# Kernel tuning notes

Hardware: AMD Instinct MI355X
Metric: run time of the kernel (lower is better)

Reference implementation:

```python
import jax, jax.numpy as jnp
import numpy as np

N_HEADS = 4
D_HEAD = 64
SCALE = D_HEAD ** -0.5


def setup_inputs() -> dict:
    key = jax.random.key(0)
    k0, k1, k2, k3, k4 = jax.random.split(key, 5)
    C = 256
    return {
        "x": jax.random.normal(k0, (32, C, 32, 32), dtype=jnp.float32),
        "W_qkv": jax.random.normal(k1, (C, 3 * N_HEADS * D_HEAD), dtype=jnp.float32) * 0.02,
        "b_qkv": jax.random.normal(k2, (3 * N_HEADS * D_HEAD,), dtype=jnp.float32) * 0.02,
        "W_out": jax.random.normal(k3, (C, C), dtype=jnp.float32) * 0.02,
        "b_out": jax.random.normal(k4, (C,), dtype=jnp.float32) * 0.02,
    }


def reference(x, W_qkv, b_qkv, W_out, b_out):
    b, c, h, w = x.shape
    # [B, C, H, W] -> [B, S, C], S = H*W  (NOTE: GroupNorm is defined in the
    # original module but never applied in forward; we match that exactly.)
    xs = x.reshape(b, c, h * w).transpose(0, 2, 1)
    qkv = (xs @ W_qkv + b_qkv).reshape(b, -1, N_HEADS, 3 * D_HEAD)
    q, k, v = jnp.split(qkv, 3, axis=-1)  # each [B, S, H, D]
    scores = jnp.einsum('bihd,bjhd->bijh', q, k) * SCALE  # [B, S, S, H]
    attn = jax.nn.softmax(scores, axis=2)  # softmax over key index j
    res = jnp.einsum('bijh,bjhd->bihd', attn, v).reshape(b, -1, N_HEADS * D_HEAD)
    res = res @ W_out + b_out + xs
    return res.transpose(0, 2, 1).reshape(b, c, h, w)
```

## Files before the change

kernel.cpp:

```cpp
#include <hip/hip_runtime.h>

#define NH 4
#define DH 64
#define SS 1024
#define CC 256
#define BB 32

typedef __attribute__((ext_vector_type(8))) short short8;
typedef __attribute__((ext_vector_type(4))) float floatx4;
typedef __attribute__((ext_vector_type(16))) float floatx16;
typedef __attribute__((ext_vector_type(2))) unsigned uint2v;

#define MFMA16(a, b, c) __builtin_amdgcn_mfma_f32_16x16x32_bf16(a, b, c, 0, 0, 0)
#define MFMA32(a, b, c) __builtin_amdgcn_mfma_f32_32x32x16_bf16(a, b, c, 0, 0, 0)

#define QSCALE 0.18033688011112042f

__device__ __forceinline__ short f2bf(float f) {
    union { float f; unsigned u; } v; v.f = f;
    unsigned r = (v.u + 0x7fffu + ((v.u >> 16) & 1u)) >> 16;
    return (short)r;
}
__device__ __forceinline__ unsigned bfrn(float f) {
    union { float f; unsigned u; } v; v.f = f;
    return (v.u + 0x7fffu + ((v.u >> 16) & 1u)) >> 16;
}
__device__ __forceinline__ unsigned pk2_trunc(float a, float b) {
    union { float f; unsigned u; } ua, ub; ua.f = a; ub.f = b;
    return (ua.u >> 16) | (ub.u & 0xFFFF0000u);
}
__device__ __forceinline__ unsigned pk2_rn(float a, float b) {
    return bfrn(a) | (bfrn(b) << 16);
}

__global__ __launch_bounds__(256) void k_prep(const float* __restrict__ x,
                                              const float* __restrict__ Wqkv,
                                              const float* __restrict__ Wout,
                                              short* __restrict__ xs,
                                              short* __restrict__ Wqkv_t,
                                              short* __restrict__ Wout_t) {
    int bid = blockIdx.x;
    if (bid < 2048) {
        __shared__ float tile[64][65];
        int b = bid >> 6;
        int s0 = ((bid >> 2) & 15) * 64;
        int c0 = (bid & 3) * 64;
        int t = threadIdx.x;
        int tx = t & 63, ty = t >> 6;
        for (int i = 0; i < 16; ++i) {
            int c = ty + i * 4;
            tile[tx][c] = x[((b * CC) + (c0 + c)) * SS + s0 + tx];
        }
        __syncthreads();
        for (int i = 0; i < 8; ++i) {
            int s = (t >> 5) + i * 8;
            int cp = (t & 31) * 2;
            short2 v;
            v.x = f2bf(tile[s][cp]);
            v.y = f2bf(tile[s][cp + 1]);
            *(short2*)(&xs[((b * SS) + (s0 + s)) * CC + c0 + cp]) = v;
        }
    } else {
        int idx = (bid - 2048) * 256 + threadIdx.x;
        if (idx < 768 * 256) {
            int n = idx >> 8, k = idx & 255;
            Wqkv_t[idx] = f2bf(Wqkv[k * 768 + n]);
        } else {
            int j = idx - 768 * 256;
            int c = j >> 8, k = j & 255;
            Wout_t[j] = f2bf(Wout[k * 256 + c]);
        }
    }
}

__global__ __launch_bounds__(256) void k_qkv(const short* __restrict__ xs,
                                             const short* __restrict__ Wt,
                                             const float* __restrict__ bqkv,
                                             short* __restrict__ qtw,
                                             short* __restrict__ kw,
                                             short* __restrict__ vtw) {
    __shared__ short smem[10240];
    short* As = smem;
    short* Bs = smem + 5120;
    int bid = blockIdx.x;
    int idx = bid >> 3;
    int m0 = ((bid & 7) * 32 + idx / 6) * 128;
    int n0 = (idx % 6) * 128;
    int t = threadIdx.x;
    int lane = t & 63, wid = t >> 6;
    int wr = wid >> 1, wc = wid & 1;
    int c16 = lane & 15, qd = lane >> 4;

    floatx4 acc[4][4] = {};
    short8 pa[2], pb[2];

    for (int j = 0; j < 2; ++j) {
        int id = j * 256 + t, row = id >> 2, cc = id & 3;
        pa[j] = *(const short8*)(&xs[(m0 + row) * CC + cc * 8]);
        pb[j] = *(const short8*)(&Wt[(n0 + row) * CC + cc * 8]);
    }
    for (int kt = 0; kt < 8; ++kt) {
        if (kt) __syncthreads();
        for (int j = 0; j < 2; ++j) {
            int id = j * 256 + t, row = id >> 2, cc = id & 3;
            *(short8*)(&As[row * 40 + cc * 8]) = pa[j];
            *(short8*)(&Bs[row * 40 + cc * 8]) = pb[j];
        }
        __syncthreads();
        if (kt < 7) {
            for (int j = 0; j < 2; ++j) {
                int id = j * 256 + t, row = id >> 2, cc = id & 3;
                pa[j] = *(const short8*)(&xs[(m0 + row) * CC + (kt + 1) * 32 + cc * 8]);
                pb[j] = *(const short8*)(&Wt[(n0 + row) * CC + (kt + 1) * 32 + cc * 8]);
            }
        }
        short8 av[4], bv[4];
        for (int i = 0; i < 4; ++i) {
            av[i] = *(const short8*)(&As[(wr * 64 + i * 16 + c16) * 40 + qd * 8]);
            bv[i] = *(const short8*)(&Bs[(wc * 64 + i * 16 + c16) * 40 + qd * 8]);
        }
        for (int mi = 0; mi < 4; ++mi)
            for (int ni = 0; ni < 4; ++ni)
                acc[mi][ni] = MFMA16(av[mi], bv[ni], acc[mi][ni]);
    }

    int b = m0 >> 10, sbase = m0 & 1023;
    int seg = (n0 >> 6) + wc;
    int sel = seg % 3, h = seg / 3;
    int bh = b * NH + h;
    float bias4[4];
    for (int ni = 0; ni < 4; ++ni)
        bias4[ni] = bqkv[n0 + wc * 64 + ni * 16 + c16];

    if (sel != 1) {
        float sc = (sel == 0) ? QSCALE : 1.f;
        short* dst = (sel == 0) ? qtw : vtw;
        for (int ni = 0; ni < 4; ++ni) {
            int d = ni * 16 + c16;
            for (int mi = 0; mi < 4; ++mi) {
                int s = sbase + wr * 64 + mi * 16 + qd * 4;
                uint2 ow;
                ow.x = pk2_rn((acc[mi][ni][0] + bias4[ni]) * sc,
                              (acc[mi][ni][1] + bias4[ni]) * sc);
                ow.y = pk2_rn((acc[mi][ni][2] + bias4[ni]) * sc,
                              (acc[mi][ni][3] + bias4[ni]) * sc);
                *(uint2*)(&dst[(size_t)(bh * DH + d) * SS + s]) = ow;
            }
        }
    }

    int seg0 = n0 >> 6;
    int kseg = (seg0 % 3 == 1) ? seg0 : (((seg0 + 1) % 3 == 1) ? seg0 + 1 : -1);
    if (kseg >= 0) {
        short* Kt = smem;
        __syncthreads();
        if (seg == kseg) {
            for (int mi = 0; mi < 4; ++mi)
                for (int ni = 0; ni < 4; ++ni)
                    for (int r = 0; r < 4; ++r)
                        Kt[(wr * 64 + mi * 16 + qd * 4 + r) * 72 + ni * 16 + c16] =
                            f2bf(acc[mi][ni][r] + bias4[ni]);
        }
        __syncthreads();
        int bhk = b * NH + kseg / 3;
        int srow = t >> 1, dh = (t & 1) * 32;
        short* gdst = &kw[(size_t)(bhk * SS + sbase + srow) * DH + dh];
        const short* lsrc = &Kt[srow * 72 + dh];
        for (int k = 0; k < 4; ++k)
            *(short8*)(gdst + k * 8) = *(const short8*)(lsrc + k * 8);
    }
}

__global__ __launch_bounds__(256) void k_attn(const short* __restrict__ qtw,
                                              const short* __restrict__ kw,
                                              const short* __restrict__ vtw,
                                              short* __restrict__ res) {
    __shared__ __align__(16) short Ks[64 * 72];
    __shared__ __align__(16) short Vts[64 * 72];
    int bid = blockIdx.x;
    int q0 = (bid >> 7) * 128;
    int bh = bid & 127;
    int t = threadIdx.x;
    int lane = t & 63, w = t >> 6;
    int l31 = lane & 31, hi = lane >> 5;
    const short* qp = qtw + (size_t)bh * DH * SS;
    const short* kp = kw + (size_t)bh * SS * DH;
    const short* vp = vtw + (size_t)bh * DH * SS;

    short8 qfrag[4];
    {
        int s = q0 + w * 32 + l31;
        for (int kd = 0; kd < 4; ++kd) {
            short8 q;
            for (int e = 0; e < 8; ++e)
                q[e] = qp[(size_t)(kd * 16 + hi * 8 + e) * SS + s];
            qfrag[kd] = q;
        }
    }

    float l_i = 0.f;
    floatx16 o_acc[2] = {};

    short8 kreg[2], vreg[2];
    for (int j = 0; j < 2; ++j) {
        int id = j * 256 + t, row = id >> 3, cc = id & 7;
        kreg[j] = *(const short8*)(&kp[row * DH + cc * 8]);
        vreg[j] = *(const short8*)(&vp[row * SS + cc * 8]);
    }

    for (int kt = 0; kt < 16; ++kt) {
        if (kt) __syncthreads();
        for (int j = 0; j < 2; ++j) {
            int id = j * 256 + t, row = id >> 3, cc = id & 7;
            *(short8*)(&Ks[row * 72 + cc * 8]) = kreg[j];
            *(short8*)(&Vts[row * 72 + cc * 8]) = vreg[j];
        }
        __syncthreads();
        if (kt < 15) {
            for (int j = 0; j < 2; ++j) {
                int id = j * 256 + t, row = id >> 3, cc = id & 7;
                kreg[j] = *(const short8*)(&kp[((kt + 1) * 64 + row) * DH + cc * 8]);
                vreg[j] = *(const short8*)(&vp[row * SS + (kt + 1) * 64 + cc * 8]);
            }
        }

#pragma unroll
        for (int jt = 0; jt < 2; ++jt) {
            short8 kf[4];
#pragma unroll
            for (int kd = 0; kd < 4; ++kd)
                kf[kd] = *(const short8*)(&Ks[(jt * 32 + l31) * 72 + kd * 16 + hi * 8]);
            short8 vf0[2], vf1[2];
#pragma unroll
            for (int dt = 0; dt < 2; ++dt) {
                vf0[dt] = *(const short8*)(&Vts[(dt * 32 + l31) * 72 + (jt * 2 + 0) * 16 + hi * 8]);
                vf1[dt] = *(const short8*)(&Vts[(dt * 32 + l31) * 72 + (jt * 2 + 1) * 16 + hi * 8]);
            }

            floatx16 sacc = {};
            __builtin_amdgcn_s_setprio(1);
#pragma unroll
            for (int kd = 0; kd < 4; ++kd)
                sacc = MFMA32(kf[kd], qfrag[kd], sacc);
            __builtin_amdgcn_s_setprio(0);

            float ls = 0.f;
            unsigned u[8];
#pragma unroll
            for (int r = 0; r < 16; r += 2) {
                float e0 = __builtin_amdgcn_exp2f(sacc[r]);
                float e1 = __builtin_amdgcn_exp2f(sacc[r + 1]);
                ls += e0 + e1;
                u[r >> 1] = pk2_trunc(e0, e1);
            }
            l_i += ls;

            uint2v r02 = __builtin_amdgcn_permlane32_swap(u[0], u[2], false, false);
            uint2v r13 = __builtin_amdgcn_permlane32_swap(u[1], u[3], false, false);
            uint2v r46 = __builtin_amdgcn_permlane32_swap(u[4], u[6], false, false);
            uint2v r57 = __builtin_amdgcn_permlane32_swap(u[5], u[7], false, false);
            union { unsigned w[4]; short8 s; } pf0, pf1;
            pf0.w[0] = r02[0]; pf0.w[1] = r13[0]; pf0.w[2] = r02[1]; pf0.w[3] = r13[1];
            pf1.w[0] = r46[0]; pf1.w[1] = r57[0]; pf1.w[2] = r46[1]; pf1.w[3] = r57[1];

            __builtin_amdgcn_s_setprio(1);
#pragma unroll
            for (int dt = 0; dt < 2; ++dt) {
                o_acc[dt] = MFMA32(vf0[dt], pf0.s, o_acc[dt]);
                o_acc[dt] = MFMA32(vf1[dt], pf1.s, o_acc[dt]);
            }
            __builtin_amdgcn_s_setprio(0);
        }
    }

    int b = bh >> 2, h = bh & 3;
    {
        float l = l_i;
        l += __shfl_xor(l, 32);
        float inv = 1.f / l;
        int s = q0 + w * 32 + l31;
        long base = (long)(b * SS + s) * CC + h * DH;
#pragma unroll
        for (int dt = 0; dt < 2; ++dt) {
#pragma unroll
            for (int q = 0; q < 4; ++q) {
                int d = dt * 32 + q * 8 + hi * 4;
                uint2 ow;
                ow.x = pk2_rn(o_acc[dt][q * 4 + 0] * inv, o_acc[dt][q * 4 + 1] * inv);
                ow.y = pk2_rn(o_acc[dt][q * 4 + 2] * inv, o_acc[dt][q * 4 + 3] * inv);
                *(uint2*)(&res[base + d]) = ow;
            }
        }
    }
}

__global__ __launch_bounds__(256) void k_out(const short* __restrict__ res,
                                             const short* __restrict__ Wot,
                                             const float* __restrict__ bout,
                                             const float* __restrict__ x,
                                             float* __restrict__ out) {
    __shared__ short As[128 * 40];
    __shared__ short Bs[128 * 40];
    int b = blockIdx.z;
    int m0 = blockIdx.y * 128;
    int n0 = blockIdx.x * 128;
    int t = threadIdx.x;
    int lane = t & 63, wid = t >> 6;
    int wr = wid >> 1, wc = wid & 1;
    int c16 = lane & 15, qd = lane >> 4;

    floatx4 acc[4][4] = {};
    short8 pa[2], pbv[2];
    for (int j = 0; j < 2; ++j) {
        int id = j * 256 + t, row = id >> 2, cc = id & 3;
        pa[j] = *(const short8*)(&Wot[(m0 + row) * CC + cc * 8]);
        pbv[j] = *(const short8*)(&res[(b * SS + n0 + row) * CC + cc * 8]);
    }

    for (int kt = 0; kt < 8; ++kt) {
        if (kt) __syncthreads();
        for (int j = 0; j < 2; ++j) {
            int id = j * 256 + t, row = id >> 2, cc = id & 3;
            *(short8*)(&As[row * 40 + cc * 8]) = pa[j];
            *(short8*)(&Bs[row * 40 + cc * 8]) = pbv[j];
        }
        __syncthreads();
        if (kt < 7) {
            for (int j = 0; j < 2; ++j) {
                int id = j * 256 + t, row = id >> 2, cc = id & 3;
                pa[j] = *(const short8*)(&Wot[(m0 + row) * CC + (kt + 1) * 32 + cc * 8]);
                pbv[j] = *(const short8*)(&res[(b * SS + n0 + row) * CC + (kt + 1) * 32 + cc * 8]);
            }
        }
        short8 av[4], bv[4];
        for (int i = 0; i < 4; ++i) {
            av[i] = *(const short8*)(&As[(wr * 64 + i * 16 + c16) * 40 + qd * 8]);
            bv[i] = *(const short8*)(&Bs[(wc * 64 + i * 16 + c16) * 40 + qd * 8]);
        }
        for (int mi = 0; mi < 4; ++mi)
            for (int ni = 0; ni < 4; ++ni)
                acc[mi][ni] = MFMA16(av[mi], bv[ni], acc[mi][ni]);
    }

    for (int mi = 0; mi < 4; ++mi) {
        for (int r = 0; r < 4; ++r) {
            int c = m0 + wr * 64 + mi * 16 + qd * 4 + r;
            float bias = bout[c];
            for (int ni = 0; ni < 4; ++ni) {
                int s = n0 + wc * 64 + ni * 16 + c16;
                float v = acc[mi][ni][r] + bias + x[((b * CC) + c) * SS + s];
                out[((b * CC) + c) * SS + s] = v;
            }
        }
    }
}

extern "C" void kernel_launch(void* const* d_in, const int* in_sizes, int n_in,
                              void* d_out, int out_size, void* d_ws, size_t ws_size,
                              hipStream_t stream) {
    const float* x    = (const float*)d_in[0];
    const float* Wqkv = (const float*)d_in[1];
    const float* bqkv = (const float*)d_in[2];
    const float* Wout = (const float*)d_in[3];
    const float* bout = (const float*)d_in[4];
    float* out = (float*)d_out;

    char* ws = (char*)d_ws;
    short* xs_res = (short*)(ws);
    short* qtw    = (short*)(ws + 16777216);
    short* kw     = (short*)(ws + 33554432);
    short* vtw    = (short*)(ws + 50331648);
    short* Wqkv_t = (short*)(ws + 67108864);
    short* Wout_t = (short*)(ws + 67502080);

    k_prep<<<dim3(3072), 256, 0, stream>>>(x, Wqkv, Wout, xs_res, Wqkv_t, Wout_t);
    k_qkv<<<dim3(1536), 256, 0, stream>>>(xs_res, Wqkv_t, bqkv, qtw, kw, vtw);
    k_attn<<<dim3(1024), 256, 0, stream>>>(qtw, kw, vtw, xs_res);
    k_out<<<dim3(8, 2, 32), 256, 0, stream>>>(xs_res, Wout_t, bout, x, out);
}
```

Before: 177.5 us.

## Load K/V MFMA fragments directly from global memory, dropping LDS staging

The attention kernel no longer stages K and V^T tiles through shared memory with register prefetch and two barriers per tile. Each wave now reads its MFMA fragments straight from global memory (relying on L1/L2 reuse across the four waves), which removes LDS traffic and __syncthreads. In exchange it loses the explicit prefetch overlap and issues four times more global load instructions, so latency exposure and cache pressure may grow.

```diff
diff --git a/kernel.cpp b/kernel.cpp
--- a/kernel.cpp
+++ b/kernel.cpp
@@ -4,7 +4,6 @@
 #define DH 64
 #define SS 1024
 #define CC 256
-#define BB 32
 
 typedef __attribute__((ext_vector_type(8))) short short8;
 typedef __attribute__((ext_vector_type(4))) float floatx4;
@@ -175,8 +174,6 @@
                                               const short* __restrict__ kw,
                                               const short* __restrict__ vtw,
                                               short* __restrict__ res) {
-    __shared__ __align__(16) short Ks[64 * 72];
-    __shared__ __align__(16) short Vts[64 * 72];
     int bid = blockIdx.x;
     int q0 = (bid >> 7) * 128;
     int bh = bid & 127;
@@ -201,40 +198,23 @@
     float l_i = 0.f;
     floatx16 o_acc[2] = {};
 
-    short8 kreg[2], vreg[2];
-    for (int j = 0; j < 2; ++j) {
-        int id = j * 256 + t, row = id >> 3, cc = id & 7;
-        kreg[j] = *(const short8*)(&kp[row * DH + cc * 8]);
-        vreg[j] = *(const short8*)(&vp[row * SS + cc * 8]);
-    }
+    const short* kfb = kp + (size_t)l31 * DH + hi * 8;
+    const short* vfb = vp + (size_t)l31 * SS + hi * 8;
 
     for (int kt = 0; kt < 16; ++kt) {
-        if (kt) __syncthreads();
-        for (int j = 0; j < 2; ++j) {
-            int id = j * 256 + t, row = id >> 3, cc = id & 7;
-            *(short8*)(&Ks[row * 72 + cc * 8]) = kreg[j];
-            *(short8*)(&Vts[row * 72 + cc * 8]) = vreg[j];
-        }
-        __syncthreads();
-        if (kt < 15) {
-            for (int j = 0; j < 2; ++j) {
-                int id = j * 256 + t, row = id >> 3, cc = id & 7;
-                kreg[j] = *(const short8*)(&kp[((kt + 1) * 64 + row) * DH + cc * 8]);
-                vreg[j] = *(const short8*)(&vp[row * SS + (kt + 1) * 64 + cc * 8]);
-            }
-        }
-
 #pragma unroll
         for (int jt = 0; jt < 2; ++jt) {
+            const short* kb = kfb + (size_t)(kt * 64 + jt * 32) * DH;
             short8 kf[4];
 #pragma unroll
             for (int kd = 0; kd < 4; ++kd)
-                kf[kd] = *(const short8*)(&Ks[(jt * 32 + l31) * 72 + kd * 16 + hi * 8]);
+                kf[kd] = *(const short8*)(kb + kd * 16);
             short8 vf0[2], vf1[2];
 #pragma unroll
             for (int dt = 0; dt < 2; ++dt) {
-                vf0[dt] = *(const short8*)(&Vts[(dt * 32 + l31) * 72 + (jt * 2 + 0) * 16 + hi * 8]);
-                vf1[dt] = *(const short8*)(&Vts[(dt * 32 + l31) * 72 + (jt * 2 + 1) * 16 + hi * 8]);
+                const short* vb = vfb + (size_t)dt * 32 * SS + kt * 64 + jt * 32;
+                vf0[dt] = *(const short8*)(vb);
+                vf1[dt] = *(const short8*)(vb + 16);
             }
 
             floatx16 sacc = {};
```

Result: slower. 277.9 us (+56.6%).
